# Optimization experiments

Hardware: AMD Instinct MI355X
Metric: run time of the kernel (lower is better)

Reference implementation:

```python
import jax, jax.numpy as jnp
import numpy as np

IN_CH = 32
HID = 2 * IN_CH          # 64
MASK_CH = 8 * 27         # 216


def conv3d(x, w, b, replicate_pad):
    # x: [B,C,D,H,W], w: [O,I,kd,kh,kw]
    if replicate_pad:
        x = jnp.pad(x, ((0, 0), (0, 0), (1, 1), (1, 1), (1, 1)), mode='edge')
    y = jax.lax.conv_general_dilated(
        x, w, window_strides=(1, 1, 1), padding='VALID',
        dimension_numbers=('NCDHW', 'OIDHW', 'NCDHW'))
    return y + b[None, :, None, None, None]


def unfold27(x):
    # replicate-padded 3x3x3 neighborhoods -> [B,C,D,H,W,27], n = kd*9+kh*3+kw
    B, C, D, H, W = x.shape
    xp = jnp.pad(x, ((0, 0), (0, 0), (1, 1), (1, 1), (1, 1)), mode='edge')
    patches = [xp[:, :, dz:dz + D, dy:dy + H, dx:dx + W]
               for dz in range(3) for dy in range(3) for dx in range(3)]
    return jnp.stack(patches, axis=-1)


def setup_inputs() -> dict:
    key = jax.random.key(0)
    ks = jax.random.split(key, 6)
    B, C, D, H, W = 1, IN_CH, 48, 48, 48
    x = jax.random.normal(ks[0], (B, C, D, H, W), dtype=jnp.float32)
    features = jax.random.normal(ks[1], (B, IN_CH, D, H, W), dtype=jnp.float32)
    # Conv(in, 2*in, k=3, replicate pad) ; Conv(2*in, 8*27, k=1, zeros pad)
    w1 = jax.random.normal(ks[2], (HID, IN_CH, 3, 3, 3), dtype=jnp.float32) * (1.0 / np.sqrt(IN_CH * 27))
    b1 = jnp.zeros((HID,), dtype=jnp.float32)
    w2 = jax.random.normal(ks[3], (MASK_CH, HID, 1, 1, 1), dtype=jnp.float32) * (1.0 / np.sqrt(HID))
    b2 = jnp.zeros((MASK_CH,), dtype=jnp.float32)
    return {"x": x, "features": features, "w1": w1, "b1": b1, "w2": w2, "b2": b2}


def reference(x, features, w1, b1, w2, b2):
    B, C, D, H, W = x.shape
    # mask network: Conv3 (replicate) -> SiLU -> Conv1 (zeros)
    h = jax.nn.silu(conv3d(features, w1, b1, replicate_pad=True))
    m = conv3d(h, w2, b2, replicate_pad=False)          # [B,216,D,H,W]
    # view(B,1,2,2,2,27,D,H,W).permute(0,1,6,2,7,3,8,4,5) -> [B,D,2,H,2,W,2,27]
    m = m.reshape(B, 2, 2, 2, 27, D, H, W)
    m = jnp.transpose(m, (0, 5, 1, 6, 2, 7, 3, 4))      # b d i h j w k n
    m = jax.nn.softmax(m, axis=-1)
    xu = unfold27(x)                                    # [B,C,D,H,W,27]
    # convex combination: contract over the 27 taps (batched small matmul)
    out = jnp.einsum('bdihjwkn,bcdhwn->bcdihjwk', m, xu)
    return out.reshape(B, C, 2 * D, 2 * H, 2 * W)
```

## Files before the change

### kernel.cpp

```cpp
#include <hip/hip_runtime.h>
#include <math.h>

#define NVOX 110592

typedef _Float16 f16x8 __attribute__((ext_vector_type(8)));
typedef _Float16 f16x4 __attribute__((ext_vector_type(4)));
typedef float    f32x4 __attribute__((ext_vector_type(4)));

__device__ __forceinline__ void fmas4(float4& a, const float4& xv, float p) {
    a.x = fmaf(xv.x, p, a.x);
    a.y = fmaf(xv.y, p, a.y);
    a.z = fmaf(xv.z, p, a.z);
    a.w = fmaf(xv.w, p, a.w);
}
__device__ __forceinline__ float comp4(const float4& v, int j) {
    return j == 0 ? v.x : (j == 1 ? v.y : (j == 2 ? v.z : v.w));
}

__global__ void k_prep(const float* __restrict__ w1, const float* __restrict__ w2,
                       _Float16* __restrict__ w1h, _Float16* __restrict__ w2h) {
    int e = blockIdx.x * 256 + threadIdx.x;
    if (e < 64 * 32 * 27) {
        int oc = e / 864;
        int r = e - oc * 864;
        int ci = r / 27;
        int tap = r - ci * 27;
        w1h[oc * 864 + tap * 32 + ci] = (_Float16)w1[e];
    }
    int e2 = e - 55296;
    if (e2 >= 0 && e2 < 224 * 64) {
        int oc = e2 >> 6, k = e2 & 63;
        w2h[e2] = (oc < 216) ? (_Float16)w2[oc * 64 + k] : (_Float16)0.f;
    }
}

__global__ __launch_bounds__(256, 4) void k_conv1(
    const float* __restrict__ feat, const _Float16* __restrict__ w1h,
    const float* __restrict__ b1, _Float16* __restrict__ hout)
{
    __shared__ _Float16 flds[9 * 50 * 40];
    int bx = blockIdx.x;
    int d = bx / 48, hh = bx - d * 48;
    int t = threadIdx.x;

    for (int i = t; i < 3600; i += 256) {
        int o = i / 450;
        int col = i - o * 450;
        int dzdy = col / 50;
        int px = col - dzdy * 50;
        int dz = dzdy / 3, dy = dzdy - dz * 3;
        int zz = min(max(d + dz - 1, 0), 47);
        int yy = min(max(hh + dy - 1, 0), 47);
        int xx = min(max(px - 1, 0), 47);
        const float* src = feat + (o * 4) * NVOX + (zz * 48 + yy) * 48 + xx;
        _Float16* dst = flds + col * 40 + o * 4;
        dst[0] = (_Float16)src[0];
        dst[1] = (_Float16)src[NVOX];
        dst[2] = (_Float16)src[2 * NVOX];
        dst[3] = (_Float16)src[3 * NVOX];
    }
    __syncthreads();

    int wid = t >> 6;
    int lane = t & 63;
    int mcol = lane & 15;
    int q = lane >> 4;

    const _Float16* wbase = w1h + (wid * 16 + mcol) * 864 + q * 8;

    f32x4 acc0 = {0.f, 0.f, 0.f, 0.f};
    f32x4 acc1 = {0.f, 0.f, 0.f, 0.f};
    f32x4 acc2 = {0.f, 0.f, 0.f, 0.f};

#pragma unroll 3
    for (int dzdy = 0; dzdy < 9; ++dzdy) {
        const _Float16* brow = flds + (dzdy * 50 + mcol) * 40 + q * 8;
        const _Float16* wrow = wbase + dzdy * 96;
#pragma unroll
        for (int dx = 0; dx < 3; ++dx) {
            f16x8 av = *(const f16x8*)(wrow + dx * 32);
            const _Float16* bb = brow + dx * 40;
            f16x8 b0 = *(const f16x8*)(bb);
            f16x8 b1v = *(const f16x8*)(bb + 16 * 40);
            f16x8 b2v = *(const f16x8*)(bb + 32 * 40);
            acc0 = __builtin_amdgcn_mfma_f32_16x16x32_f16(av, b0, acc0, 0, 0, 0);
            acc1 = __builtin_amdgcn_mfma_f32_16x16x32_f16(av, b1v, acc1, 0, 0, 0);
            acc2 = __builtin_amdgcn_mfma_f32_16x16x32_f16(av, b2v, acc2, 0, 0, 0);
        }
    }

    __syncthreads();
    _Float16* transh = flds;
    float4 bv = ((const float4*)b1)[wid * 4 + q];
    {
        f32x4 accs[3] = {acc0, acc1, acc2};
#pragma unroll
        for (int p = 0; p < 3; ++p) {
            int px = p * 16 + mcol;
            f16x4 o;
            float s;
            s = accs[p][0] + bv.x; o.x = (_Float16)(s / (1.f + __expf(-s)));
            s = accs[p][1] + bv.y; o.y = (_Float16)(s / (1.f + __expf(-s)));
            s = accs[p][2] + bv.z; o.z = (_Float16)(s / (1.f + __expf(-s)));
            s = accs[p][3] + bv.w; o.w = (_Float16)(s / (1.f + __expf(-s)));
            *(f16x4*)(transh + px * 72 + wid * 16 + q * 4) = o;
        }
    }
    __syncthreads();
    for (int i = t; i < 384; i += 256) {
        int c = i & 7, px = i >> 3;
        f16x8 v = *(const f16x8*)(transh + px * 72 + c * 8);
        ((f16x8*)hout)[(bx * 48 + px) * 8 + c] = v;
    }
}

__global__ __launch_bounds__(256, 2) void k_fused(
    const float* __restrict__ x, const _Float16* __restrict__ hws,
    const _Float16* __restrict__ w2h, const float* __restrict__ b2,
    float* __restrict__ out)
{
    __shared__ float smem[13800];
    float4* smem4 = (float4*)smem;
    _Float16* hl = (_Float16*)(smem + 5376);
    int bx = blockIdx.x;
    int d = bx / 96;
    int r = bx - d * 96;
    int hh = r >> 1;
    int w0 = (r & 1) * 24;
    int t = threadIdx.x;
    int vox0 = (d * 48 + hh) * 48 + w0;

    if (t < 192) {
        int vox = t >> 3, c = t & 7;
        *(f16x8*)(hl + vox * 72 + c * 8) = ((const f16x8*)hws)[(vox0 + vox) * 8 + c];
    } else {
        int i = t - 192;
        int vox = 24 + (i >> 3), c = i & 7;
        f16x8 z = {0, 0, 0, 0, 0, 0, 0, 0};
        *(f16x8*)(hl + vox * 72 + c * 8) = z;
    }
    __syncthreads();

    {
        int wid = t >> 6, lane = t & 63;
        int mcol = lane & 15, q = lane >> 4;
        for (int mt = wid; mt < 14; mt += 4) {
            float bias[4];
#pragma unroll
            for (int rr = 0; rr < 4; ++rr) {
                int oc = mt * 16 + q * 4 + rr;
                bias[rr] = (oc < 216) ? b2[oc] : 0.f;
            }
            f32x4 acc0 = {bias[0], bias[1], bias[2], bias[3]};
            f32x4 acc1 = acc0;
#pragma unroll
            for (int ks = 0; ks < 2; ++ks) {
                f16x8 av = *(const f16x8*)(w2h + (mt * 16 + mcol) * 64 + ks * 32 + q * 8);
                f16x8 bv0 = *(const f16x8*)(hl + mcol * 72 + ks * 32 + q * 8);
                f16x8 bv1 = *(const f16x8*)(hl + (16 + mcol) * 72 + ks * 32 + q * 8);
                acc0 = __builtin_amdgcn_mfma_f32_16x16x32_f16(av, bv0, acc0, 0, 0, 0);
                acc1 = __builtin_amdgcn_mfma_f32_16x16x32_f16(av, bv1, acc1, 0, 0, 0);
            }
#pragma unroll
            for (int rr = 0; rr < 4; ++rr) {
                int oc = mt * 16 + q * 4 + rr;
                if (oc < 216) {
                    int sub = oc / 27;
                    int n = oc - sub * 27;
                    smem[(sub * 24 + mcol) * 28 + n] = acc0[rr];
                    int vox1 = 16 + mcol;
                    if (vox1 < 24)
                        smem[(sub * 24 + vox1) * 28 + n] = acc1[rr];
                }
            }
        }
    }
    __syncthreads();

    for (int i = t; i < 1872; i += 256) {
        int cq = i / 234;
        int col = i - cq * 234;
        int dzdy = col / 26;
        int px = col - dzdy * 26;
        int dz = dzdy / 3, dy = dzdy - dz * 3;
        int zz = min(max(d + dz - 1, 0), 47);
        int yy = min(max(hh + dy - 1, 0), 47);
        int xx = min(max(w0 + px - 1, 0), 47);
        const float* src = x + (cq * 4) * NVOX + (zz * 48 + yy) * 48 + xx;
        float4 v;
        v.x = src[0];
        v.y = src[NVOX];
        v.z = src[2 * NVOX];
        v.w = src[3 * NVOX];
        smem4[1344 + col * 9 + cq] = v;
    }
    if (t < 192) {
        int sub = t / 24;
        int vox = t - sub * 24;
        float* p = smem + (sub * 24 + vox) * 28;
        float mx = p[0];
#pragma unroll
        for (int n = 1; n < 27; ++n) mx = fmaxf(mx, p[n]);
        float s = 0.f;
#pragma unroll
        for (int n = 0; n < 27; ++n) { float e = __expf(p[n] - mx); p[n] = e; s += e; }
        float inv = 1.f / s;
#pragma unroll
        for (int n = 0; n < 27; ++n) p[n] *= inv;
    }
    __syncthreads();

    int tx = t & 7, ty = t >> 3;
    int cq = ty & 7, sp = ty >> 3;
    float4 acc[2][3];
#pragma unroll
    for (int s = 0; s < 2; ++s)
#pragma unroll
        for (int wi = 0; wi < 3; ++wi)
            acc[s][wi] = make_float4(0.f, 0.f, 0.f, 0.f);

#pragma unroll
    for (int g = 0; g < 7; ++g) {
        float4 p4[2][3];
#pragma unroll
        for (int s = 0; s < 2; ++s)
#pragma unroll
            for (int wi = 0; wi < 3; ++wi)
                p4[s][wi] = smem4[((sp * 2 + s) * 24 + tx + wi * 8) * 7 + g];
#pragma unroll
        for (int j = 0; j < 4; ++j) {
            int n = g * 4 + j;
            if (n < 27) {
                int dz = n / 9;
                int rem = n - dz * 9;
                int dy = rem / 3, dx = rem - dy * 3;
#pragma unroll
                for (int wi = 0; wi < 3; ++wi) {
                    float4 xv = smem4[1344 + ((dz * 3 + dy) * 26 + tx + wi * 8 + dx) * 9 + cq];
                    fmas4(acc[0][wi], xv, comp4(p4[0][wi], j));
                    fmas4(acc[1][wi], xv, comp4(p4[1][wi], j));
                }
            }
        }
    }

    int i_ = sp >> 1, j_ = sp & 1;
    int rowz = 2 * d + i_;
    int rowy = 2 * hh + j_;
#pragma unroll
    for (int wi = 0; wi < 3; ++wi) {
        int wg = w0 + tx + wi * 8;
#pragma unroll
        for (int cc = 0; cc < 4; ++cc) {
            int c = cq * 4 + cc;
            float2 v;
            v.x = comp4(acc[0][wi], cc);
            v.y = comp4(acc[1][wi], cc);
            *(float2*)(out + (((size_t)c * 96 + rowz) * 96 + rowy) * 96 + 2 * wg) = v;
        }
    }
}

extern "C" void kernel_launch(void* const* d_in, const int* in_sizes, int n_in,
                              void* d_out, int out_size, void* d_ws, size_t ws_size,
                              hipStream_t stream) {
    const float* x    = (const float*)d_in[0];
    const float* feat = (const float*)d_in[1];
    const float* w1   = (const float*)d_in[2];
    const float* b1   = (const float*)d_in[3];
    const float* w2   = (const float*)d_in[4];
    const float* b2   = (const float*)d_in[5];
    float* out = (float*)d_out;

    _Float16* w1h = (_Float16*)d_ws;
    _Float16* w2h = (_Float16*)((char*)d_ws + 110592);
    _Float16* hws = (_Float16*)((char*)d_ws + 139264);

    k_prep<<<272, 256, 0, stream>>>(w1, w2, w1h, w2h);
    k_conv1<<<2304, 256, 0, stream>>>(feat, w1h, b1, hws);
    k_fused<<<4608, 256, 0, stream>>>(x, hws, w2h, b2, out);
}
```

Baseline: 285.1 us.

## Pre-transpose feat and x to channel-last fp16 for vectorized halo loads

Adds a k_prepT kernel that converts feat and x from NCDHW fp32 into voxel-major fp16 buffers with 32 contiguous channels per voxel. k_conv1 and k_fused then fill their halo tiles with 16-byte vector loads instead of four strided scalar loads per element. k_fused keeps its x tile in fp16 in shared memory, which shrinks LDS so occupancy can go from 2 to 4 blocks per CU, and its softmax is rewritten to use float4 register loads. The cost is an extra kernel launch, an extra round trip of the transposed data through memory, and x rounded to fp16 in the final convex combination, which loses accuracy.

```diff
diff --git a/kernel.cpp b/kernel.cpp
--- a/kernel.cpp
+++ b/kernel.cpp
@@ -5,6 +5,7 @@
 
 typedef _Float16 f16x8 __attribute__((ext_vector_type(8)));
 typedef _Float16 f16x4 __attribute__((ext_vector_type(4)));
+typedef _Float16 f16x2 __attribute__((ext_vector_type(2)));
 typedef float    f32x4 __attribute__((ext_vector_type(4)));
 
 __device__ __forceinline__ void fmas4(float4& a, const float4& xv, float p) {
@@ -34,30 +35,53 @@
     }
 }
 
+__global__ __launch_bounds__(256) void k_prepT(
+    const float* __restrict__ feat, const float* __restrict__ x,
+    _Float16* __restrict__ featT, _Float16* __restrict__ xT)
+{
+    __shared__ _Float16 tile[64 * 36];
+    int bx = blockIdx.x;
+    int which = bx >= 1728;
+    int v0 = (which ? bx - 1728 : bx) * 64;
+    const float* s = which ? x : feat;
+    _Float16* dt = which ? xT : featT;
+    int t = threadIdx.x;
+
+    for (int i = t; i < 1024; i += 256) {
+        int c2 = i >> 6, dv = i & 63;
+        f16x2 v;
+        v.x = (_Float16)s[(2 * c2) * NVOX + v0 + dv];
+        v.y = (_Float16)s[(2 * c2 + 1) * NVOX + v0 + dv];
+        *(f16x2*)(tile + dv * 36 + c2 * 2) = v;
+    }
+    __syncthreads();
+    for (int i = t; i < 512; i += 256) {
+        int dv = i >> 3, ch = i & 7;
+        f16x4 v = *(const f16x4*)(tile + dv * 36 + ch * 4);
+        *(f16x4*)(dt + (v0 + dv) * 32 + ch * 4) = v;
+    }
+}
+
 __global__ __launch_bounds__(256, 4) void k_conv1(
-    const float* __restrict__ feat, const _Float16* __restrict__ w1h,
+    const _Float16* __restrict__ featT, const _Float16* __restrict__ w1h,
     const float* __restrict__ b1, _Float16* __restrict__ hout)
 {
-    __shared__ _Float16 flds[9 * 50 * 40];
+    __shared__ _Float16 flds[450 * 40];
     int bx = blockIdx.x;
     int d = bx / 48, hh = bx - d * 48;
     int t = threadIdx.x;
 
-    for (int i = t; i < 3600; i += 256) {
-        int o = i / 450;
-        int col = i - o * 450;
+    for (int i = t; i < 1800; i += 256) {
+        int col = i >> 2, chunk = i & 3;
         int dzdy = col / 50;
         int px = col - dzdy * 50;
         int dz = dzdy / 3, dy = dzdy - dz * 3;
         int zz = min(max(d + dz - 1, 0), 47);
         int yy = min(max(hh + dy - 1, 0), 47);
         int xx = min(max(px - 1, 0), 47);
-        const float* src = feat + (o * 4) * NVOX + (zz * 48 + yy) * 48 + xx;
-        _Float16* dst = flds + col * 40 + o * 4;
-        dst[0] = (_Float16)src[0];
-        dst[1] = (_Float16)src[NVOX];
-        dst[2] = (_Float16)src[2 * NVOX];
-        dst[3] = (_Float16)src[3 * NVOX];
+        int vox = (zz * 48 + yy) * 48 + xx;
+        *(f16x8*)(flds + col * 40 + chunk * 8) =
+            *(const f16x8*)(featT + vox * 32 + chunk * 8);
     }
     __syncthreads();
 
@@ -114,14 +138,14 @@
     }
 }
 
-__global__ __launch_bounds__(256, 2) void k_fused(
-    const float* __restrict__ x, const _Float16* __restrict__ hws,
+__global__ __launch_bounds__(256, 4) void k_fused(
+    const _Float16* __restrict__ xT, const _Float16* __restrict__ hws,
     const _Float16* __restrict__ w2h, const float* __restrict__ b2,
     float* __restrict__ out)
 {
-    __shared__ float smem[13800];
-    float4* smem4 = (float4*)smem;
+    __shared__ float smem[10056];
     _Float16* hl = (_Float16*)(smem + 5376);
+    _Float16* xh = (_Float16*)(smem + 5376);
     int bx = blockIdx.x;
     int d = bx / 96;
     int r = bx - d * 96;
@@ -177,39 +201,50 @@
     }
     __syncthreads();
 
-    for (int i = t; i < 1872; i += 256) {
-        int cq = i / 234;
-        int col = i - cq * 234;
+    for (int i = t; i < 936; i += 256) {
+        int col = i >> 2, chunk = i & 3;
         int dzdy = col / 26;
         int px = col - dzdy * 26;
         int dz = dzdy / 3, dy = dzdy - dz * 3;
         int zz = min(max(d + dz - 1, 0), 47);
         int yy = min(max(hh + dy - 1, 0), 47);
         int xx = min(max(w0 + px - 1, 0), 47);
-        const float* src = x + (cq * 4) * NVOX + (zz * 48 + yy) * 48 + xx;
-        float4 v;
-        v.x = src[0];
-        v.y = src[NVOX];
-        v.z = src[2 * NVOX];
-        v.w = src[3 * NVOX];
-        smem4[1344 + col * 9 + cq] = v;
+        int vox = (zz * 48 + yy) * 48 + xx;
+        *(f16x8*)(xh + col * 40 + chunk * 8) =
+            *(const f16x8*)(xT + vox * 32 + chunk * 8);
     }
     if (t < 192) {
         int sub = t / 24;
         int vox = t - sub * 24;
-        float* p = smem + (sub * 24 + vox) * 28;
-        float mx = p[0];
-#pragma unroll
-        for (int n = 1; n < 27; ++n) mx = fmaxf(mx, p[n]);
+        float4* p4p = (float4*)(smem + (sub * 24 + vox) * 28);
+        float4 v[7];
+#pragma unroll
+        for (int g = 0; g < 7; ++g) v[g] = p4p[g];
+        float mx = fmaxf(fmaxf(v[6].x, v[6].y), v[6].z);
+#pragma unroll
+        for (int g = 0; g < 6; ++g)
+            mx = fmaxf(mx, fmaxf(fmaxf(v[g].x, v[g].y), fmaxf(v[g].z, v[g].w)));
         float s = 0.f;
 #pragma unroll
-        for (int n = 0; n < 27; ++n) { float e = __expf(p[n] - mx); p[n] = e; s += e; }
+        for (int g = 0; g < 7; ++g) {
+            v[g].x = __expf(v[g].x - mx);
+            v[g].y = __expf(v[g].y - mx);
+            v[g].z = __expf(v[g].z - mx);
+            v[g].w = __expf(v[g].w - mx);
+        }
+        v[6].w = 0.f;
+#pragma unroll
+        for (int g = 0; g < 7; ++g) s += v[g].x + v[g].y + v[g].z + v[g].w;
         float inv = 1.f / s;
 #pragma unroll
-        for (int n = 0; n < 27; ++n) p[n] *= inv;
-    }
-    __syncthreads();
-
+        for (int g = 0; g < 7; ++g) {
+            v[g].x *= inv; v[g].y *= inv; v[g].z *= inv; v[g].w *= inv;
+            p4p[g] = v[g];
+        }
+    }
+    __syncthreads();
+
+    float4* smem4 = (float4*)smem;
     int tx = t & 7, ty = t >> 3;
     int cq = ty & 7, sp = ty >> 3;
     float4 acc[2][3];
@@ -236,7 +271,10 @@
                 int dy = rem / 3, dx = rem - dy * 3;
 #pragma unroll
                 for (int wi = 0; wi < 3; ++wi) {
-                    float4 xv = smem4[1344 + ((dz * 3 + dy) * 26 + tx + wi * 8 + dx) * 9 + cq];
+                    int col = (dz * 3 + dy) * 26 + tx + wi * 8 + dx;
+                    f16x4 xr = *(const f16x4*)(xh + col * 40 + cq * 4);
+                    float4 xv = make_float4((float)xr.x, (float)xr.y,
+                                            (float)xr.z, (float)xr.w);
                     fmas4(acc[0][wi], xv, comp4(p4[0][wi], j));
                     fmas4(acc[1][wi], xv, comp4(p4[1][wi], j));
                 }
@@ -272,11 +310,14 @@
     const float* b2   = (const float*)d_in[5];
     float* out = (float*)d_out;
 
-    _Float16* w1h = (_Float16*)d_ws;
-    _Float16* w2h = (_Float16*)((char*)d_ws + 110592);
-    _Float16* hws = (_Float16*)((char*)d_ws + 139264);
+    _Float16* w1h   = (_Float16*)d_ws;
+    _Float16* w2h   = (_Float16*)((char*)d_ws + 110592);
+    _Float16* featT = (_Float16*)((char*)d_ws + 139264);
+    _Float16* xT    = (_Float16*)((char*)d_ws + 7217152);
+    _Float16* hws   = (_Float16*)((char*)d_ws + 14295040);
 
     k_prep<<<272, 256, 0, stream>>>(w1, w2, w1h, w2h);
-    k_conv1<<<2304, 256, 0, stream>>>(feat, w1h, b1, hws);
-    k_fused<<<4608, 256, 0, stream>>>(x, hws, w2h, b2, out);
-}
+    k_prepT<<<3456, 256, 0, stream>>>(feat, x, featT, xT);
+    k_conv1<<<2304, 256, 0, stream>>>(featT, w1h, b1, hws);
+    k_fused<<<4608, 256, 0, stream>>>(xT, hws, w2h, b2, out);
+}
```

New measurement: 262.1 us. -8.1%, faster.
